# Kernel tuning notes

Hardware: AMD Instinct MI355X
Metric: run time of the kernel (lower is better)

## Reference

```python
import math
import jax, jax.numpy as jnp
import numpy as np

N_HEADS = 16
HIDDEN = 1024
FACTOR = 256
N_DK = HIDDEN // N_HEADS
B, S = 4, 2048


def _linear_params(key, fan_in, fan_out):
    kw, kb = jax.random.split(key)
    bound = 1.0 / math.sqrt(fan_in)
    W = jax.random.uniform(kw, (fan_in, fan_out), jnp.float32, -bound, bound)
    b = jax.random.uniform(kb, (fan_out,), jnp.float32, -bound, bound)
    return W, b


def setup_inputs() -> dict:
    key = jax.random.key(0)
    ks = jax.random.split(key, 12)
    inp = {
        "query": jax.random.normal(ks[0], (B, S, HIDDEN), jnp.float32),
        "key": jax.random.normal(ks[1], (B, S, HIDDEN), jnp.float32),
        "value": jax.random.normal(ks[2], (B, S, HIDDEN), jnp.float32),
        "mask": jax.random.randint(ks[3], (B, S), 0, 2, jnp.int32),
    }
    names = [("pq", HIDDEN, FACTOR), ("tq", FACTOR, HIDDEN),
             ("pk", HIDDEN, FACTOR), ("tk", FACTOR, HIDDEN),
             ("pv", HIDDEN, FACTOR), ("tv", FACTOR, HIDDEN),
             ("po", HIDDEN, FACTOR), ("to", FACTOR, HIDDEN)]
    for i, (nm, fi, fo) in enumerate(names):
        W, b = _linear_params(ks[4 + i], fi, fo)
        inp[f"W{nm}"], inp[f"b{nm}"] = W, b
    return inp


def _factored(x, Wp, bp, Wt, bt):
    # proj -> leaky_relu(0.2) -> tran
    h = jax.nn.leaky_relu(x @ Wp + bp, negative_slope=0.2)
    return h @ Wt + bt


def reference(query, key, value, mask,
              Wpq, bpq, Wtq, btq, Wpk, bpk, Wtk, btk,
              Wpv, bpv, Wtv, btv, Wpo, bpo, Wto, bto):
    bsize = query.shape[0]

    def split_heads(x):  # [B,S,H*Dk] -> [B,H,S,Dk]
        return x.reshape(bsize, -1, N_HEADS, N_DK).transpose(0, 2, 1, 3)

    q = split_heads(_factored(query, Wpq, bpq, Wtq, btq))
    k = split_heads(_factored(key, Wpk, bpk, Wtk, btk))
    v = split_heads(_factored(value, Wpv, bpv, Wtv, btv))

    scores = jnp.einsum("bhqd,bhkd->bhqk", q, k) / math.sqrt(N_DK)
    m = (mask == 0)[:, None, None, :]  # [B,1,1,S]
    scores = jnp.where(m, jnp.float32(-1e20), scores)
    attn = jax.nn.softmax(scores, axis=-1)
    cv = jnp.einsum("bhqk,bhkd->bhqd", attn, v)
    cv = cv.transpose(0, 2, 1, 3).reshape(bsize, -1, N_HEADS * N_DK)
    # dropout omitted (eval mode / deterministic reference)
    return _factored(cv, Wpo, bpo, Wto, bto)
```

## Files before the change

### kernel.cpp

```cpp
#include <hip/hip_runtime.h>
#include <cstdint>
#include <cstddef>

typedef __bf16 bf16_t;
typedef __bf16 bf16x8 __attribute__((ext_vector_type(8)));
typedef float  f32x4  __attribute__((ext_vector_type(4)));
typedef unsigned int uint32x4 __attribute__((ext_vector_type(4)));
typedef unsigned int uint32x2 __attribute__((ext_vector_type(2)));

#define DEV_INLINE __device__ __forceinline__

constexpr int Bsz = 4, Ssz = 2048, HID = 1024, FAC = 256, NH = 16, DKc = 64;
constexpr int Mrows = Bsz * Ssz;
constexpr float QSCALE = 0.18033688011112042f;

struct Ptr8 { const float* p[8]; };
struct Ptr3 { const float* p[3]; };

DEV_INLINE float fast_exp2(float x) {
#if __has_builtin(__builtin_amdgcn_exp2f)
  return __builtin_amdgcn_exp2f(x);
#else
  return exp2f(x);
#endif
}

DEV_INLINE void async16(const void* g, void* l) {
  __builtin_amdgcn_global_load_lds((const __attribute__((address_space(1))) void*)g,
                                   (__attribute__((address_space(3))) void*)l, 16, 0, 0);
}

DEV_INLINE int SW(int r) { return (r & 3) | ((r >> 1) & 4); }

__global__ __launch_bounds__(256) void k_prep(Ptr8 w, Ptr8 bsrc, const int* __restrict__ mask,
                                              bf16_t* wpt, bf16_t* wtt,
                                              float* bp, float* bt, float* mf, bf16_t* mb) {
  const int z = blockIdx.z;
  if (z == 8) {
    const int bid = blockIdx.y * 32 + blockIdx.x;
    if (bid >= 64) return;
    const int i = bid * 256 + threadIdx.x;
    if (i < 4 * FAC) bp[i] = bsrc.p[i >> 8][i & 255];
    if (i < 4 * HID) bt[i] = bsrc.p[4 + (i >> 10)][i & 1023];
    if (i < Bsz * Ssz) {
      const float m = (mask[i] != 0) ? 1.f : 0.f;
      mf[i] = m;
      mb[i] = (bf16_t)m;
    }
    return;
  }
  const int K = (z < 4) ? HID : FAC;
  const int N = (z < 4) ? FAC : HID;
  if ((int)(blockIdx.x * 32) >= N || (int)(blockIdx.y * 32) >= K) return;
  __shared__ float t[32][33];
  const float* src = w.p[z];
  bf16_t* dst = (z < 4) ? (wpt + (size_t)z * FAC * HID) : (wtt + (size_t)(z - 4) * FAC * HID);
  const int tx = threadIdx.x & 31, ty = threadIdx.x >> 5;
  const int kb = blockIdx.y * 32, nb = blockIdx.x * 32;
#pragma unroll
  for (int j = 0; j < 4; ++j)
    t[ty + j * 8][tx] = src[(size_t)(kb + ty + j * 8) * N + nb + tx];
  __syncthreads();
#pragma unroll
  for (int j = 0; j < 4; ++j)
    dst[(size_t)(nb + ty + j * 8) * K + kb + tx] = (bf16_t)t[tx][ty + j * 8];
}

template <int CAST_A, typename OUT_T>
__global__ __launch_bounds__(256) void k_gemmP(Ptr3 Asrc,
                                               const bf16_t* __restrict__ Aall,
                                               const bf16_t* __restrict__ Bt_,
                                               const float* __restrict__ biasAll,
                                               OUT_T* __restrict__ Call,
                                               int K,
                                               long long Az, long long Bz, long long Cz, int biasz) {
  constexpr int LDTA = CAST_A ? 40 : 32;
  __shared__ __align__(16) bf16_t As[2][64 * LDTA];
  __shared__ __align__(16) bf16_t Bs[2][128 * 32];

  const int z = blockIdx.z;
  const bf16_t* Bt = Bt_ + (size_t)z * Bz;
  const float* bias = biasAll + (size_t)z * biasz;
  OUT_T* C = Call + (size_t)z * Cz;

  const int tid = threadIdx.x;
  const int lane = tid & 63, wave = tid >> 6;
  const int quad = lane >> 4, l16 = lane & 15;
  const int m0 = blockIdx.y * 64, n0 = blockIdx.x * 128;

  const int arow = wave * 16 + (lane >> 2), akc = (lane & 3) * 8;
  const bf16_t* gB0 = Bt + (size_t)(n0 + arow) * K + akc;
  const bf16_t* gB1 = gB0 + (size_t)64 * K;

  const float* gAf = nullptr;
  const bf16_t* gA = nullptr;
  const int crow = tid >> 2, chalf = (tid & 3) * 8;
  if (CAST_A) gAf = Asrc.p[z] + (size_t)(m0 + crow) * K + chalf;
  else        gA  = Aall + (size_t)z * Az + (size_t)(m0 + arow) * K + akc;

  async16(gB0, Bs[0] + wave * 512);
  async16(gB1, Bs[0] + 2048 + wave * 512);
  if (CAST_A) {
    f32x4 x0 = *(const f32x4*)gAf;
    f32x4 x1 = *(const f32x4*)(gAf + 4);
    union { bf16_t h[8]; uint32x4 u; } o;
#pragma unroll
    for (int j = 0; j < 4; ++j) { o.h[j] = (bf16_t)x0[j]; o.h[4 + j] = (bf16_t)x1[j]; }
    *(uint32x4*)(As[0] + crow * LDTA + chalf) = o.u;
  } else {
    async16(gA, As[0] + wave * 512);
  }

  f32x4 acc[4][2] = {};
  const int nk = K / 32;

  for (int it = 0; it < nk; ++it) {
    const int cur = it & 1, nxt = cur ^ 1;
    __syncthreads();

    f32x4 xa, xb;
    const int k1 = (it + 1) * 32;
    if (it + 1 < nk) {
      async16(gB0 + k1, Bs[nxt] + wave * 512);
      async16(gB1 + k1, Bs[nxt] + 2048 + wave * 512);
      if (CAST_A) {
        xa = *(const f32x4*)(gAf + k1);
        xb = *(const f32x4*)(gAf + k1 + 4);
      } else {
        async16(gA + k1, As[nxt] + wave * 512);
      }
    }

    bf16x8 af[4], bfr[2];
#pragma unroll
    for (int i = 0; i < 4; ++i)
      af[i] = *(const bf16x8*)(As[cur] + (i * 16 + l16) * LDTA + quad * 8);
#pragma unroll
    for (int i = 0; i < 2; ++i)
      bfr[i] = *(const bf16x8*)(Bs[cur] + (wave * 32 + i * 16 + l16) * 32 + quad * 8);
#pragma unroll
    for (int mi = 0; mi < 4; ++mi)
#pragma unroll
      for (int ni = 0; ni < 2; ++ni)
        acc[mi][ni] = __builtin_amdgcn_mfma_f32_16x16x32_bf16(af[mi], bfr[ni], acc[mi][ni], 0, 0, 0);

    if (CAST_A && it + 1 < nk) {
      union { bf16_t h[8]; uint32x4 u; } o;
#pragma unroll
      for (int j = 0; j < 4; ++j) { o.h[j] = (bf16_t)xa[j]; o.h[4 + j] = (bf16_t)xb[j]; }
      *(uint32x4*)(As[nxt] + crow * LDTA + chalf) = o.u;
    }
  }

#pragma unroll
  for (int mi = 0; mi < 4; ++mi) {
    const int rbase = m0 + mi * 16 + quad * 4;
#pragma unroll
    for (int ni = 0; ni < 2; ++ni) {
      const int col = n0 + wave * 32 + ni * 16 + l16;
      const float bv = bias[col];
#pragma unroll
      for (int r = 0; r < 4; ++r) {
        float y = acc[mi][ni][r] + bv;
        y = (y > 0.f) ? y : 0.2f * y;
        C[(size_t)(rbase + r) * FAC + col] = (OUT_T)y;
      }
    }
  }
}

template <int TVW, typename OUT_T>
__global__ __launch_bounds__(256) void k_gemm(const bf16_t* __restrict__ Aall,
                                              const bf16_t* __restrict__ Btall,
                                              const float* __restrict__ biasAll,
                                              OUT_T* __restrict__ Call,
                                              bf16_t* __restrict__ C2,
                                              const float* __restrict__ rowmul,
                                              int N, int K,
                                              long long Az, long long Bz, long long Cz, int biasz,
                                              float sc0, float sc1) {
  __shared__ __align__(16) bf16_t As[2][128 * 32];
  __shared__ __align__(16) bf16_t Bs[2][128 * 32];

  const int z = blockIdx.z;
  const bf16_t* Bt = Btall + (size_t)z * Bz;
  const float* bias = biasAll + (size_t)z * biasz;
  OUT_T* C = Call + (size_t)z * Cz;
  const float scale = (z == 0) ? sc0 : sc1;

  const int tid = threadIdx.x;
  const int lane = tid & 63, wave = tid >> 6;
  const int quad = lane >> 4, l16 = lane & 15;
  const int wr = wave >> 1, wc = wave & 1;
  const int m0 = blockIdx.y * 128, n0 = blockIdx.x * 128;

  const int arow = wave * 16 + (lane >> 2), akc = (lane & 3) * 8;
  const bf16_t* gB0 = Bt + (size_t)(n0 + arow) * K + akc;
  const bf16_t* gB1 = gB0 + (size_t)64 * K;
  const bf16_t* A = Aall + (size_t)z * Az;
  const bf16_t* gA0 = A + (size_t)(m0 + arow) * K + akc;
  const bf16_t* gA1 = gA0 + (size_t)64 * K;

  async16(gB0, Bs[0] + wave * 512);
  async16(gB1, Bs[0] + 2048 + wave * 512);
  async16(gA0, As[0] + wave * 512);
  async16(gA1, As[0] + 2048 + wave * 512);

  f32x4 acc[4][4] = {};
  const int nk = K / 32;

  for (int it = 0; it < nk; ++it) {
    const int cur = it & 1, nxt = cur ^ 1;
    __syncthreads();

    if (it + 1 < nk) {
      const int k1 = (it + 1) * 32;
      async16(gB0 + k1, Bs[nxt] + wave * 512);
      async16(gB1 + k1, Bs[nxt] + 2048 + wave * 512);
      async16(gA0 + k1, As[nxt] + wave * 512);
      async16(gA1 + k1, As[nxt] + 2048 + wave * 512);
    }

    bf16x8 af[4], bfr[4];
#pragma unroll
    for (int i = 0; i < 4; ++i)
      af[i] = *(const bf16x8*)(As[cur] + (wr * 64 + i * 16 + l16) * 32 + quad * 8);
#pragma unroll
    for (int i = 0; i < 4; ++i)
      bfr[i] = *(const bf16x8*)(Bs[cur] + (wc * 64 + i * 16 + l16) * 32 + quad * 8);
#pragma unroll
    for (int mi = 0; mi < 4; ++mi)
#pragma unroll
      for (int ni = 0; ni < 4; ++ni)
        acc[mi][ni] = __builtin_amdgcn_mfma_f32_16x16x32_bf16(af[mi], bfr[ni], acc[mi][ni], 0, 0, 0);
  }

  if (TVW && z == 2) {
#pragma unroll
    for (int mi = 0; mi < 4; ++mi) {
      const int rbase = m0 + wr * 64 + mi * 16 + quad * 4;
      const int bb = rbase >> 11, s = rbase & 2047;
      float rmv[4];
#pragma unroll
      for (int r = 0; r < 4; ++r) rmv[r] = rowmul[rbase + r];
#pragma unroll
      for (int ni = 0; ni < 4; ++ni) {
        const int col = n0 + wc * 64 + ni * 16 + l16;
        const float bv = bias[col];
        const int h = col >> 6, d = col & 63;
        union { bf16_t e[4]; uint32x2 u; } p;
#pragma unroll
        for (int r = 0; r < 4; ++r) p.e[r] = (bf16_t)((acc[mi][ni][r] + bv) * rmv[r]);
        *(uint32x2*)(C2 + (((size_t)((bb * NH + h) * DKc + d)) << 11) + s) = p.u;
      }
    }
    return;
  }

#pragma unroll
  for (int mi = 0; mi < 4; ++mi) {
    const int rbase = m0 + wr * 64 + mi * 16 + quad * 4;
#pragma unroll
    for (int ni = 0; ni < 4; ++ni) {
      const int col = n0 + wc * 64 + ni * 16 + l16;
      const float bv = bias[col];
#pragma unroll
      for (int r = 0; r < 4; ++r) {
        float y = (acc[mi][ni][r] + bv) * scale;
        C[(size_t)(rbase + r) * N + col] = (OUT_T)y;
      }
    }
  }
}

__global__ __launch_bounds__(512, 4) void k_attn(const bf16_t* __restrict__ qkv,
                                                 const bf16_t* __restrict__ mb,
                                                 bf16_t* __restrict__ cv) {
  __shared__ __align__(16) bf16_t Ks[2][64 * 64];
  __shared__ __align__(16) bf16_t Vt[2][64 * 64];
  __shared__ __align__(16) bf16_t Ml[Ssz];

  const int qt = blockIdx.x, h = blockIdx.y, b = blockIdx.z;
  const bf16_t* qp = qkv;
  const bf16_t* kp = qkv + (size_t)Mrows * HID;
  const bf16_t* vtp = qkv + 2 * (size_t)Mrows * HID + (size_t)(b * NH + h) * DKc * Ssz;

  const int tid = threadIdx.x;
  const int lane = tid & 63, wave = tid >> 6;
  const int quad = lane >> 4, l16 = lane & 15;

  const int r0 = wave * 8 + (lane >> 3);
  const int c0 = ((lane & 7) ^ SW(r0)) * 8;
  const int ldsOff = wave * 512;
  const bf16_t* kgA = kp + (size_t)(b * Ssz + r0) * HID + h * DKc + c0;
  const bf16_t* vgA = vtp + (size_t)r0 * Ssz + c0;

  *(uint32x2*)(Ml + tid * 4) = *(const uint32x2*)(mb + (size_t)b * Ssz + tid * 4);
  async16(kgA, Ks[0] + ldsOff);
  async16(vgA, Vt[0] + ldsOff);

  bf16x8 aq0[2], aq1[2];
#pragma unroll
  for (int g = 0; g < 2; ++g) {
    const size_t qrow = (size_t)(b * Ssz + qt * 256 + g * 128 + wave * 16 + l16) * HID + h * DKc + quad * 8;
    aq0[g] = *(const bf16x8*)(qp + qrow);
    aq1[g] = *(const bf16x8*)(qp + qrow + 32);
  }
  __syncthreads();

  const int krow = 8 * (l16 >> 2) + (l16 & 3);
  f32x4 acc[2][4] = {};
  f32x4 dacc[2] = {};
  const bf16x8 zfrag = {};

  for (int kt = 0; kt < 32; ++kt) {
    const int cur = kt & 1, nxt = cur ^ 1;
    if (kt < 31) {
      const size_t ko = (size_t)(kt + 1) * 64 * HID;
      const int vo = (kt + 1) * 64;
      async16(kgA + ko, Ks[nxt] + ldsOff);
      async16(vgA + vo, Vt[nxt] + ldsOff);
    }

    union U { uint32x4 u; bf16x8 h; } ap0[2], ap1[2];
    constexpr int koff[4] = {0, 4, 32, 36};
#pragma unroll
    for (int ks = 0; ks < 4; ++ks) {
      const int row = krow + koff[ks];
      const int sw = SW(row);
      bf16x8 a0 = *(const bf16x8*)(Ks[cur] + row * 64 + (quad ^ sw) * 8);
      bf16x8 a1 = *(const bf16x8*)(Ks[cur] + row * 64 + ((quad + 4) ^ sw) * 8);
#pragma unroll
      for (int g = 0; g < 2; ++g) {
        f32x4 c = {};
        c = __builtin_amdgcn_mfma_f32_16x16x32_bf16(a0, aq0[g], c, 0, 0, 0);
        c = __builtin_amdgcn_mfma_f32_16x16x32_bf16(a1, aq1[g], c, 0, 0, 0);
        union { bf16_t h[2]; uint32_t u; } p01, p23;
        p01.h[0] = (bf16_t)fast_exp2(c[0]);
        p01.h[1] = (bf16_t)fast_exp2(c[1]);
        p23.h[0] = (bf16_t)fast_exp2(c[2]);
        p23.h[1] = (bf16_t)fast_exp2(c[3]);
        U& t = (ks < 2) ? ap0[g] : ap1[g];
        t.u[(ks & 1) * 2] = p01.u;
        t.u[(ks & 1) * 2 + 1] = p23.u;
      }
    }

    bf16x8 mr0 = *(const bf16x8*)(Ml + kt * 64 + quad * 8);
    bf16x8 mr1 = *(const bf16x8*)(Ml + kt * 64 + 32 + quad * 8);
    if (l16 != 0) { mr0 = zfrag; mr1 = zfrag; }
#pragma unroll
    for (int g = 0; g < 2; ++g) {
      dacc[g] = __builtin_amdgcn_mfma_f32_16x16x32_bf16(ap0[g].h, mr0, dacc[g], 0, 0, 0);
      dacc[g] = __builtin_amdgcn_mfma_f32_16x16x32_bf16(ap1[g].h, mr1, dacc[g], 0, 0, 0);
    }

#pragma unroll
    for (int d = 0; d < 4; ++d) {
      const int row = d * 16 + l16;
      const int sw = SW(row);
      bf16x8 bv0 = *(const bf16x8*)(Vt[cur] + row * 64 + (quad ^ sw) * 8);
      bf16x8 bv1 = *(const bf16x8*)(Vt[cur] + row * 64 + ((quad + 4) ^ sw) * 8);
#pragma unroll
      for (int g = 0; g < 2; ++g) {
        acc[g][d] = __builtin_amdgcn_mfma_f32_16x16x32_bf16(ap0[g].h, bv0, acc[g][d], 0, 0, 0);
        acc[g][d] = __builtin_amdgcn_mfma_f32_16x16x32_bf16(ap1[g].h, bv1, acc[g][d], 0, 0, 0);
      }
    }

    __syncthreads();
  }

#pragma unroll
  for (int g = 0; g < 2; ++g) {
    const size_t obase = (size_t)(b * Ssz + qt * 256 + g * 128 + wave * 16 + quad * 4) * HID + h * DKc + l16;
#pragma unroll
    for (int r = 0; r < 4; ++r) {
      const float denom = __shfl(dacc[g][r], lane & 48, 64);
      const float rl = 1.f / denom;
#pragma unroll
      for (int d = 0; d < 4; ++d)
        cv[obase + (size_t)r * HID + d * 16] = (bf16_t)(acc[g][d][r] * rl);
    }
  }
}

extern "C" void kernel_launch(void* const* d_in, const int* in_sizes, int n_in,
                              void* d_out, int out_size, void* d_ws, size_t ws_size,
                              hipStream_t stream) {
  (void)in_sizes; (void)n_in; (void)out_size; (void)ws_size;
  const float* q_in = (const float*)d_in[0];
  const float* k_in = (const float*)d_in[1];
  const float* v_in = (const float*)d_in[2];
  const int* mask = (const int*)d_in[3];

  bf16_t* XB = (bf16_t*)d_ws;
  bf16_t* H3 = XB + (size_t)3 * Mrows * HID;
  bf16_t* CV = H3 + (size_t)3 * Mrows * FAC;
  bf16_t* WPT = CV + (size_t)Mrows * HID;
  bf16_t* WTT = WPT + (size_t)4 * FAC * HID;
  float* BP = (float*)(WTT + (size_t)4 * FAC * HID);
  float* BT = BP + 4 * FAC;
  float* MF = BT + 4 * HID;
  bf16_t* MB = (bf16_t*)(MF + Mrows);
  bf16_t* VTg = XB + 2 * (size_t)Mrows * HID;

  Ptr8 w;
  w.p[0] = (const float*)d_in[4];  w.p[1] = (const float*)d_in[8];
  w.p[2] = (const float*)d_in[12]; w.p[3] = (const float*)d_in[16];
  w.p[4] = (const float*)d_in[6];  w.p[5] = (const float*)d_in[10];
  w.p[6] = (const float*)d_in[14]; w.p[7] = (const float*)d_in[18];
  Ptr8 bs;
  bs.p[0] = (const float*)d_in[5];  bs.p[1] = (const float*)d_in[9];
  bs.p[2] = (const float*)d_in[13]; bs.p[3] = (const float*)d_in[17];
  bs.p[4] = (const float*)d_in[7];  bs.p[5] = (const float*)d_in[11];
  bs.p[6] = (const float*)d_in[15]; bs.p[7] = (const float*)d_in[19];
  hipLaunchKernelGGL(k_prep, dim3(32, 32, 9), dim3(256), 0, stream, w, bs, mask,
                     WPT, WTT, BP, BT, MF, MB);

  Ptr3 xs; xs.p[0] = q_in; xs.p[1] = k_in; xs.p[2] = v_in;
  Ptr3 nullp; nullp.p[0] = nullp.p[1] = nullp.p[2] = nullptr;

  hipLaunchKernelGGL((k_gemmP<1, bf16_t>), dim3(2, Mrows / 64, 3), dim3(256), 0, stream,
                     xs, (const bf16_t*)nullptr, WPT, BP, H3,
                     HID, 0LL, (long long)FAC * HID, (long long)Mrows * FAC, FAC);

  hipLaunchKernelGGL((k_gemm<1, bf16_t>), dim3(HID / 128, Mrows / 128, 3), dim3(256), 0, stream,
                     H3, WTT, BT, XB, VTg, MF,
                     HID, FAC, (long long)Mrows * FAC, (long long)FAC * HID, (long long)Mrows * HID, HID,
                     QSCALE, 1.f);

  hipLaunchKernelGGL(k_attn, dim3(Ssz / 256, NH, Bsz), dim3(512), 0, stream, XB, MB, CV);

  hipLaunchKernelGGL((k_gemmP<0, bf16_t>), dim3(2, Mrows / 64, 1), dim3(256), 0, stream,
                     nullp, CV, WPT + (size_t)3 * FAC * HID, BP + 3 * FAC, H3,
                     HID, 0LL, 0LL, 0LL, 0);

  hipLaunchKernelGGL((k_gemm<0, float>), dim3(HID / 128, Mrows / 128, 1), dim3(256), 0, stream,
                     H3, WTT + (size_t)3 * FAC * HID, BT + 3 * HID, (float*)d_out, (bf16_t*)nullptr,
                     (const float*)nullptr, HID, FAC, 0LL, 0LL, 0LL, 0, 1.f, 1.f);
}
```

Measured before the change: 340.6 us.

## Split attention key tiles across two wave teams with LDS reduction

Waves are now split into two teams. Each team handles half of every 64-key tile (32 keys) for all 64 query rows, where previously each wave covered 32 query rows across the full key tile. At the end, team 1 writes its partial accumulators and denominators to a new LDS scratch buffer, and team 0 adds them and writes the normalized output. The aim is to halve the per-wave K fragment loads and exp work per query row, and to change register usage. The cost is more accumulator registers, extra LDS (about 20KB), and a final reduction with several barriers, which could lower occupancy.

After: 656.0 us. 92.6% more time.

```diff
diff --git a/kernel.cpp b/kernel.cpp
--- a/kernel.cpp
+++ b/kernel.cpp
@@ -279,6 +279,7 @@
   __shared__ __align__(16) bf16_t Ks[2][64 * 64];
   __shared__ __align__(16) bf16_t Vt[2][64 * 64];
   __shared__ __align__(16) bf16_t Ml[Ssz];
+  __shared__ __align__(16) float scr[256 * 20];
 
   const int qt = blockIdx.x, h = blockIdx.y, b = blockIdx.z;
   const bf16_t* qp = qkv;
@@ -288,6 +289,7 @@
   const int tid = threadIdx.x;
   const int lane = tid & 63, wave = tid >> 6;
   const int quad = lane >> 4, l16 = lane & 15;
+  const int team = wave >> 2, w4 = wave & 3;
 
   const int r0 = wave * 8 + (lane >> 3);
   const int c0 = ((lane & 7) ^ SW(r0)) * 8;
@@ -299,18 +301,18 @@
   async16(kgA, Ks[0] + ldsOff);
   async16(vgA, Vt[0] + ldsOff);
 
-  bf16x8 aq0[2], aq1[2];
-#pragma unroll
-  for (int g = 0; g < 2; ++g) {
-    const size_t qrow = (size_t)(b * Ssz + qt * 256 + g * 128 + wave * 16 + l16) * HID + h * DKc + quad * 8;
+  bf16x8 aq0[4], aq1[4];
+#pragma unroll
+  for (int g = 0; g < 4; ++g) {
+    const size_t qrow = (size_t)(b * Ssz + qt * 256 + g * 64 + w4 * 16 + l16) * HID + h * DKc + quad * 8;
     aq0[g] = *(const bf16x8*)(qp + qrow);
     aq1[g] = *(const bf16x8*)(qp + qrow + 32);
   }
   __syncthreads();
 
   const int krow = 8 * (l16 >> 2) + (l16 & 3);
-  f32x4 acc[2][4] = {};
-  f32x4 dacc[2] = {};
+  f32x4 acc[4][4] = {};
+  f32x4 dacc[4] = {};
   const bf16x8 zfrag = {};
 
   for (int kt = 0; kt < 32; ++kt) {
@@ -322,16 +324,15 @@
       async16(vgA + vo, Vt[nxt] + ldsOff);
     }
 
-    union U { uint32x4 u; bf16x8 h; } ap0[2], ap1[2];
-    constexpr int koff[4] = {0, 4, 32, 36};
-#pragma unroll
-    for (int ks = 0; ks < 4; ++ks) {
-      const int row = krow + koff[ks];
+    union U { uint32x4 u; bf16x8 h; } ap[4];
+#pragma unroll
+    for (int ks = 0; ks < 2; ++ks) {
+      const int row = krow + ks * 4 + team * 32;
       const int sw = SW(row);
       bf16x8 a0 = *(const bf16x8*)(Ks[cur] + row * 64 + (quad ^ sw) * 8);
       bf16x8 a1 = *(const bf16x8*)(Ks[cur] + row * 64 + ((quad + 4) ^ sw) * 8);
 #pragma unroll
-      for (int g = 0; g < 2; ++g) {
+      for (int g = 0; g < 4; ++g) {
         f32x4 c = {};
         c = __builtin_amdgcn_mfma_f32_16x16x32_bf16(a0, aq0[g], c, 0, 0, 0);
         c = __builtin_amdgcn_mfma_f32_16x16x32_bf16(a1, aq1[g], c, 0, 0, 0);
@@ -340,48 +341,53 @@
         p01.h[1] = (bf16_t)fast_exp2(c[1]);
         p23.h[0] = (bf16_t)fast_exp2(c[2]);
         p23.h[1] = (bf16_t)fast_exp2(c[3]);
-        U& t = (ks < 2) ? ap0[g] : ap1[g];
-        t.u[(ks & 1) * 2] = p01.u;
-        t.u[(ks & 1) * 2 + 1] = p23.u;
-      }
-    }
-
-    bf16x8 mr0 = *(const bf16x8*)(Ml + kt * 64 + quad * 8);
-    bf16x8 mr1 = *(const bf16x8*)(Ml + kt * 64 + 32 + quad * 8);
-    if (l16 != 0) { mr0 = zfrag; mr1 = zfrag; }
-#pragma unroll
-    for (int g = 0; g < 2; ++g) {
-      dacc[g] = __builtin_amdgcn_mfma_f32_16x16x32_bf16(ap0[g].h, mr0, dacc[g], 0, 0, 0);
-      dacc[g] = __builtin_amdgcn_mfma_f32_16x16x32_bf16(ap1[g].h, mr1, dacc[g], 0, 0, 0);
-    }
+        ap[g].u[ks * 2] = p01.u;
+        ap[g].u[ks * 2 + 1] = p23.u;
+      }
+    }
+
+    bf16x8 mr = *(const bf16x8*)(Ml + kt * 64 + team * 32 + quad * 8);
+    if (l16 != 0) mr = zfrag;
+#pragma unroll
+    for (int g = 0; g < 4; ++g)
+      dacc[g] = __builtin_amdgcn_mfma_f32_16x16x32_bf16(ap[g].h, mr, dacc[g], 0, 0, 0);
 
 #pragma unroll
     for (int d = 0; d < 4; ++d) {
       const int row = d * 16 + l16;
       const int sw = SW(row);
-      bf16x8 bv0 = *(const bf16x8*)(Vt[cur] + row * 64 + (quad ^ sw) * 8);
-      bf16x8 bv1 = *(const bf16x8*)(Vt[cur] + row * 64 + ((quad + 4) ^ sw) * 8);
-#pragma unroll
-      for (int g = 0; g < 2; ++g) {
-        acc[g][d] = __builtin_amdgcn_mfma_f32_16x16x32_bf16(ap0[g].h, bv0, acc[g][d], 0, 0, 0);
-        acc[g][d] = __builtin_amdgcn_mfma_f32_16x16x32_bf16(ap1[g].h, bv1, acc[g][d], 0, 0, 0);
-      }
+      bf16x8 bv = *(const bf16x8*)(Vt[cur] + row * 64 + (((quad + team * 4)) ^ sw) * 8);
+#pragma unroll
+      for (int g = 0; g < 4; ++g)
+        acc[g][d] = __builtin_amdgcn_mfma_f32_16x16x32_bf16(ap[g].h, bv, acc[g][d], 0, 0, 0);
     }
 
     __syncthreads();
   }
 
-#pragma unroll
-  for (int g = 0; g < 2; ++g) {
-    const size_t obase = (size_t)(b * Ssz + qt * 256 + g * 128 + wave * 16 + quad * 4) * HID + h * DKc + l16;
-#pragma unroll
-    for (int r = 0; r < 4; ++r) {
-      const float denom = __shfl(dacc[g][r], lane & 48, 64);
-      const float rl = 1.f / denom;
-#pragma unroll
-      for (int d = 0; d < 4; ++d)
-        cv[obase + (size_t)r * HID + d * 16] = (bf16_t)(acc[g][d][r] * rl);
-    }
+  const int sbase = (w4 * 64 + lane) * 20;
+  for (int g = 0; g < 4; ++g) {
+    if (team == 1) {
+#pragma unroll
+      for (int d = 0; d < 4; ++d) *(f32x4*)(scr + sbase + d * 4) = acc[g][d];
+      *(f32x4*)(scr + sbase + 16) = dacc[g];
+    }
+    __syncthreads();
+    if (team == 0) {
+#pragma unroll
+      for (int d = 0; d < 4; ++d) acc[g][d] += *(const f32x4*)(scr + sbase + d * 4);
+      dacc[g] += *(const f32x4*)(scr + sbase + 16);
+      const size_t obase = (size_t)(b * Ssz + qt * 256 + g * 64 + w4 * 16 + quad * 4) * HID + h * DKc + l16;
+#pragma unroll
+      for (int r = 0; r < 4; ++r) {
+        const float denom = __shfl(dacc[g][r], lane & 48, 64);
+        const float rl = 1.f / denom;
+#pragma unroll
+        for (int d = 0; d < 4; ++d)
+          cv[obase + (size_t)r * HID + d * 16] = (bf16_t)(acc[g][d][r] * rl);
+      }
+    }
+    __syncthreads();
   }
 }
 
```

## Fuse factored proj and tran GEMMs into one kernel keeping hidden tile in LDS

Applied to the files above, without the earlier changes.

Replaces the separate projection GEMM (K=1024 to 256) and transform GEMM (256 to 1024) with one 512-thread kernel per 64-row tile. The leaky-ReLU intermediate stays in shared memory and is never written to or read back from global memory, and the launch count drops from four GEMM launches to two. In exchange each block computes all 1024 output columns serially in 32 chunks. The grid shrinks to 128 blocks per z, which lowers parallelism, and the larger LDS footprint may reduce occupancy.

Result: no change. 343.7 us (+0.9%).

```diff
diff --git a/kernel.cpp b/kernel.cpp
--- a/kernel.cpp
+++ b/kernel.cpp
@@ -66,211 +66,183 @@
     dst[(size_t)(nb + ty + j * 8) * K + kb + tx] = (bf16_t)t[tx][ty + j * 8];
 }
 
-template <int CAST_A, typename OUT_T>
-__global__ __launch_bounds__(256) void k_gemmP(Ptr3 Asrc,
-                                               const bf16_t* __restrict__ Aall,
-                                               const bf16_t* __restrict__ Bt_,
-                                               const float* __restrict__ biasAll,
-                                               OUT_T* __restrict__ Call,
-                                               int K,
-                                               long long Az, long long Bz, long long Cz, int biasz) {
+template <int CAST_A, int QKV, typename OUT_T>
+__global__ __launch_bounds__(512, 4) void k_fact(Ptr3 Asrc, const bf16_t* __restrict__ Abf,
+                                                 const bf16_t* __restrict__ WpAll,
+                                                 const float* __restrict__ bpAll,
+                                                 const bf16_t* __restrict__ WtAll,
+                                                 const float* __restrict__ btAll,
+                                                 OUT_T* __restrict__ CoutAll,
+                                                 bf16_t* __restrict__ C2,
+                                                 const float* __restrict__ rowmul) {
   constexpr int LDTA = CAST_A ? 40 : 32;
-  __shared__ __align__(16) bf16_t As[2][64 * LDTA];
-  __shared__ __align__(16) bf16_t Bs[2][128 * 32];
-
-  const int z = blockIdx.z;
-  const bf16_t* Bt = Bt_ + (size_t)z * Bz;
-  const float* bias = biasAll + (size_t)z * biasz;
-  OUT_T* C = Call + (size_t)z * Cz;
+  __shared__ __align__(16) bf16_t smem[2 * 64 * 40 + 2 * 256 * 32 + 64 * 264];
+  bf16_t* As  = smem;
+  bf16_t* Bs1 = smem + 2 * 64 * 40;
+  bf16_t* Bs2 = smem;
+  bf16_t* Hl  = smem + 2 * 64 * 40 + 2 * 256 * 32;
+
+  const int z = QKV ? blockIdx.z : 3;
+  const bf16_t* Wp = WpAll + (size_t)z * FAC * HID;
+  const float* bp = bpAll + z * FAC;
+  const bf16_t* Wt = WtAll + (size_t)z * FAC * HID;
+  const float* bt = btAll + z * HID;
+  OUT_T* Cout = QKV ? (CoutAll + (size_t)blockIdx.z * Mrows * HID) : CoutAll;
 
   const int tid = threadIdx.x;
   const int lane = tid & 63, wave = tid >> 6;
   const int quad = lane >> 4, l16 = lane & 15;
-  const int m0 = blockIdx.y * 64, n0 = blockIdx.x * 128;
-
-  const int arow = wave * 16 + (lane >> 2), akc = (lane & 3) * 8;
-  const bf16_t* gB0 = Bt + (size_t)(n0 + arow) * K + akc;
-  const bf16_t* gB1 = gB0 + (size_t)64 * K;
-
+  const int m0 = blockIdx.x * 64;
+
+  const int b1row = wave * 32 + (lane >> 2), b1col = (lane & 3) * 8;
+  const bf16_t* gW0 = Wp + (size_t)b1row * HID + b1col;
+  const bf16_t* gW1 = gW0 + (size_t)16 * HID;
+  bf16_t* lW0 = Bs1 + wave * 1024;
+  bf16_t* lW1 = lW0 + 512;
+
+  const int ar = tid >> 3, acf = (tid & 7) * 4;
   const float* gAf = nullptr;
-  const bf16_t* gA = nullptr;
-  const int crow = tid >> 2, chalf = (tid & 3) * 8;
-  if (CAST_A) gAf = Asrc.p[z] + (size_t)(m0 + crow) * K + chalf;
-  else        gA  = Aall + (size_t)z * Az + (size_t)(m0 + arow) * K + akc;
-
-  async16(gB0, Bs[0] + wave * 512);
-  async16(gB1, Bs[0] + 2048 + wave * 512);
+  const bf16_t* gAb = nullptr;
+  bf16_t* lA = As + wave * 512;
+  if (CAST_A) gAf = Asrc.p[z] + (size_t)(m0 + ar) * HID + acf;
+  else        gAb = Abf + (size_t)(m0 + wave * 16 + (lane >> 2)) * HID + (lane & 3) * 8;
+
+  async16(gW0, lW0);
+  async16(gW1, lW1);
   if (CAST_A) {
-    f32x4 x0 = *(const f32x4*)gAf;
-    f32x4 x1 = *(const f32x4*)(gAf + 4);
-    union { bf16_t h[8]; uint32x4 u; } o;
-#pragma unroll
-    for (int j = 0; j < 4; ++j) { o.h[j] = (bf16_t)x0[j]; o.h[4 + j] = (bf16_t)x1[j]; }
-    *(uint32x4*)(As[0] + crow * LDTA + chalf) = o.u;
-  } else {
-    async16(gA, As[0] + wave * 512);
+    f32x4 x = *(const f32x4*)gAf;
+    union { bf16_t h[4]; uint32x2 u; } o;
+#pragma unroll
+    for (int j = 0; j < 4; ++j) o.h[j] = (bf16_t)x[j];
+    *(uint32x2*)(As + ar * LDTA + acf) = o.u;
+  } else if (wave < 4) {
+    async16(gAb, lA);
   }
 
   f32x4 acc[4][2] = {};
-  const int nk = K / 32;
-
-  for (int it = 0; it < nk; ++it) {
+
+  for (int it = 0; it < 32; ++it) {
     const int cur = it & 1, nxt = cur ^ 1;
     __syncthreads();
 
-    f32x4 xa, xb;
-    const int k1 = (it + 1) * 32;
-    if (it + 1 < nk) {
-      async16(gB0 + k1, Bs[nxt] + wave * 512);
-      async16(gB1 + k1, Bs[nxt] + 2048 + wave * 512);
-      if (CAST_A) {
-        xa = *(const f32x4*)(gAf + k1);
-        xb = *(const f32x4*)(gAf + k1 + 4);
-      } else {
-        async16(gA + k1, As[nxt] + wave * 512);
-      }
+    f32x4 xa = {};
+    if (it + 1 < 32) {
+      const int k1 = (it + 1) * 32;
+      async16(gW0 + k1, lW0 + nxt * 8192);
+      async16(gW1 + k1, lW1 + nxt * 8192);
+      if (CAST_A) xa = *(const f32x4*)(gAf + k1);
+      else if (wave < 4) async16(gAb + k1, lA + nxt * 2048);
     }
 
     bf16x8 af[4], bfr[2];
 #pragma unroll
     for (int i = 0; i < 4; ++i)
-      af[i] = *(const bf16x8*)(As[cur] + (i * 16 + l16) * LDTA + quad * 8);
+      af[i] = *(const bf16x8*)(As + cur * 64 * LDTA + (i * 16 + l16) * LDTA + quad * 8);
 #pragma unroll
     for (int i = 0; i < 2; ++i)
-      bfr[i] = *(const bf16x8*)(Bs[cur] + (wave * 32 + i * 16 + l16) * 32 + quad * 8);
+      bfr[i] = *(const bf16x8*)(Bs1 + cur * 8192 + (wave * 32 + i * 16 + l16) * 32 + quad * 8);
 #pragma unroll
     for (int mi = 0; mi < 4; ++mi)
 #pragma unroll
       for (int ni = 0; ni < 2; ++ni)
         acc[mi][ni] = __builtin_amdgcn_mfma_f32_16x16x32_bf16(af[mi], bfr[ni], acc[mi][ni], 0, 0, 0);
 
-    if (CAST_A && it + 1 < nk) {
-      union { bf16_t h[8]; uint32x4 u; } o;
-#pragma unroll
-      for (int j = 0; j < 4; ++j) { o.h[j] = (bf16_t)xa[j]; o.h[4 + j] = (bf16_t)xb[j]; }
-      *(uint32x4*)(As[nxt] + crow * LDTA + chalf) = o.u;
-    }
-  }
-
-#pragma unroll
-  for (int mi = 0; mi < 4; ++mi) {
-    const int rbase = m0 + mi * 16 + quad * 4;
+    if (CAST_A && it + 1 < 32) {
+      union { bf16_t h[4]; uint32x2 u; } o;
+#pragma unroll
+      for (int j = 0; j < 4; ++j) o.h[j] = (bf16_t)xa[j];
+      *(uint32x2*)(As + nxt * 64 * LDTA + ar * LDTA + acf) = o.u;
+    }
+  }
+
+#pragma unroll
+  for (int mi = 0; mi < 4; ++mi)
 #pragma unroll
     for (int ni = 0; ni < 2; ++ni) {
-      const int col = n0 + wave * 32 + ni * 16 + l16;
-      const float bv = bias[col];
+      const int col = wave * 32 + ni * 16 + l16;
+      const float bv = bp[col];
 #pragma unroll
       for (int r = 0; r < 4; ++r) {
         float y = acc[mi][ni][r] + bv;
         y = (y > 0.f) ? y : 0.2f * y;
-        C[(size_t)(rbase + r) * FAC + col] = (OUT_T)y;
+        Hl[(mi * 16 + quad * 4 + r) * 264 + col] = (bf16_t)y;
       }
-    }
-  }
-}
-
-template <int TVW, typename OUT_T>
-__global__ __launch_bounds__(256) void k_gemm(const bf16_t* __restrict__ Aall,
-                                              const bf16_t* __restrict__ Btall,
-                                              const float* __restrict__ biasAll,
-                                              OUT_T* __restrict__ Call,
-                                              bf16_t* __restrict__ C2,
-                                              const float* __restrict__ rowmul,
-                                              int N, int K,
-                                              long long Az, long long Bz, long long Cz, int biasz,
-                                              float sc0, float sc1) {
-  __shared__ __align__(16) bf16_t As[2][128 * 32];
-  __shared__ __align__(16) bf16_t Bs[2][128 * 32];
-
-  const int z = blockIdx.z;
-  const bf16_t* Bt = Btall + (size_t)z * Bz;
-  const float* bias = biasAll + (size_t)z * biasz;
-  OUT_T* C = Call + (size_t)z * Cz;
-  const float scale = (z == 0) ? sc0 : sc1;
-
-  const int tid = threadIdx.x;
-  const int lane = tid & 63, wave = tid >> 6;
-  const int quad = lane >> 4, l16 = lane & 15;
-  const int wr = wave >> 1, wc = wave & 1;
-  const int m0 = blockIdx.y * 128, n0 = blockIdx.x * 128;
-
-  const int arow = wave * 16 + (lane >> 2), akc = (lane & 3) * 8;
-  const bf16_t* gB0 = Bt + (size_t)(n0 + arow) * K + akc;
-  const bf16_t* gB1 = gB0 + (size_t)64 * K;
-  const bf16_t* A = Aall + (size_t)z * Az;
-  const bf16_t* gA0 = A + (size_t)(m0 + arow) * K + akc;
-  const bf16_t* gA1 = gA0 + (size_t)64 * K;
-
-  async16(gB0, Bs[0] + wave * 512);
-  async16(gB1, Bs[0] + 2048 + wave * 512);
-  async16(gA0, As[0] + wave * 512);
-  async16(gA1, As[0] + 2048 + wave * 512);
-
-  f32x4 acc[4][4] = {};
-  const int nk = K / 32;
-
-  for (int it = 0; it < nk; ++it) {
-    const int cur = it & 1, nxt = cur ^ 1;
+      acc[mi][ni] = (f32x4){0.f, 0.f, 0.f, 0.f};
+    }
+  __syncthreads();
+
+  const int b2row = wave * 32 + (lane >> 2), b2col = (lane & 3) * 8;
+#define STAGE2(ci, buf)                                                                  \
+  {                                                                                      \
+    const int nb_ = ((ci) >> 3) * 256, k0_ = ((ci) & 7) * 32;                            \
+    const bf16_t* g0_ = Wt + (size_t)(nb_ + b2row) * FAC + k0_ + b2col;                  \
+    async16(g0_, Bs2 + (buf) * 8192 + wave * 1024);                                      \
+    async16(g0_ + 16 * FAC, Bs2 + (buf) * 8192 + wave * 1024 + 512);                     \
+  }
+  STAGE2(0, 0);
+
+  for (int ci = 0; ci < 32; ++ci) {
+    const int cur = ci & 1, nxt = cur ^ 1;
     __syncthreads();
-
-    if (it + 1 < nk) {
-      const int k1 = (it + 1) * 32;
-      async16(gB0 + k1, Bs[nxt] + wave * 512);
-      async16(gB1 + k1, Bs[nxt] + 2048 + wave * 512);
-      async16(gA0 + k1, As[nxt] + wave * 512);
-      async16(gA1 + k1, As[nxt] + 2048 + wave * 512);
-    }
-
-    bf16x8 af[4], bfr[4];
+    if (ci + 1 < 32) STAGE2(ci + 1, nxt);
+
+    bf16x8 af[4], bfr[2];
+    const int k0 = (ci & 7) * 32;
 #pragma unroll
     for (int i = 0; i < 4; ++i)
-      af[i] = *(const bf16x8*)(As[cur] + (wr * 64 + i * 16 + l16) * 32 + quad * 8);
-#pragma unroll
-    for (int i = 0; i < 4; ++i)
-      bfr[i] = *(const bf16x8*)(Bs[cur] + (wc * 64 + i * 16 + l16) * 32 + quad * 8);
+      af[i] = *(const bf16x8*)(Hl + (i * 16 + l16) * 264 + k0 + quad * 8);
+#pragma unroll
+    for (int i = 0; i < 2; ++i)
+      bfr[i] = *(const bf16x8*)(Bs2 + cur * 8192 + (wave * 32 + i * 16 + l16) * 32 + quad * 8);
 #pragma unroll
     for (int mi = 0; mi < 4; ++mi)
 #pragma unroll
-      for (int ni = 0; ni < 4; ++ni)
+      for (int ni = 0; ni < 2; ++ni)
         acc[mi][ni] = __builtin_amdgcn_mfma_f32_16x16x32_bf16(af[mi], bfr[ni], acc[mi][ni], 0, 0, 0);
-  }
-
-  if (TVW && z == 2) {
-#pragma unroll
-    for (int mi = 0; mi < 4; ++mi) {
-      const int rbase = m0 + wr * 64 + mi * 16 + quad * 4;
-      const int bb = rbase >> 11, s = rbase & 2047;
-      float rmv[4];
-#pragma unroll
-      for (int r = 0; r < 4; ++r) rmv[r] = rowmul[rbase + r];
-#pragma unroll
-      for (int ni = 0; ni < 4; ++ni) {
-        const int col = n0 + wc * 64 + ni * 16 + l16;
-        const float bv = bias[col];
-        const int h = col >> 6, d = col & 63;
-        union { bf16_t e[4]; uint32x2 u; } p;
-#pragma unroll
-        for (int r = 0; r < 4; ++r) p.e[r] = (bf16_t)((acc[mi][ni][r] + bv) * rmv[r]);
-        *(uint32x2*)(C2 + (((size_t)((bb * NH + h) * DKc + d)) << 11) + s) = p.u;
+
+    if ((ci & 7) == 7) {
+      const int nbase = (ci >> 3) * 256;
+      if (QKV && blockIdx.z == 2) {
+#pragma unroll
+        for (int mi = 0; mi < 4; ++mi) {
+          const int rbase = m0 + mi * 16 + quad * 4;
+          const int bb = rbase >> 11, s = rbase & 2047;
+          float rmv[4];
+#pragma unroll
+          for (int r = 0; r < 4; ++r) rmv[r] = rowmul[rbase + r];
+#pragma unroll
+          for (int ni = 0; ni < 2; ++ni) {
+            const int col = nbase + wave * 32 + ni * 16 + l16;
+            const float bv = bt[col];
+            const int hh = col >> 6, d = col & 63;
+            union { bf16_t e[4]; uint32x2 u; } p;
+#pragma unroll
+            for (int r = 0; r < 4; ++r) p.e[r] = (bf16_t)((acc[mi][ni][r] + bv) * rmv[r]);
+            *(uint32x2*)(C2 + (((size_t)((bb * NH + hh) * DKc + d)) << 11) + s) = p.u;
+          }
+        }
+      } else {
+        const float scale = (QKV && blockIdx.z == 0) ? QSCALE : 1.f;
+#pragma unroll
+        for (int mi = 0; mi < 4; ++mi) {
+          const int row = m0 + mi * 16 + quad * 4;
+#pragma unroll
+          for (int ni = 0; ni < 2; ++ni) {
+            const int col = nbase + wave * 32 + ni * 16 + l16;
+            const float bv = bt[col];
+#pragma unroll
+            for (int r = 0; r < 4; ++r)
+              Cout[(size_t)(row + r) * HID + col] = (OUT_T)((acc[mi][ni][r] + bv) * scale);
+          }
+        }
       }
-    }
-    return;
-  }
-
-#pragma unroll
-  for (int mi = 0; mi < 4; ++mi) {
-    const int rbase = m0 + wr * 64 + mi * 16 + quad * 4;
-#pragma unroll
-    for (int ni = 0; ni < 4; ++ni) {
-      const int col = n0 + wc * 64 + ni * 16 + l16;
-      const float bv = bias[col];
-#pragma unroll
-      for (int r = 0; r < 4; ++r) {
-        float y = (acc[mi][ni][r] + bv) * scale;
-        C[(size_t)(rbase + r) * N + col] = (OUT_T)y;
-      }
-    }
-  }
+#pragma unroll
+      for (int mi = 0; mi < 4; ++mi)
+#pragma unroll
+        for (int ni = 0; ni < 2; ++ni) acc[mi][ni] = (f32x4){0.f, 0.f, 0.f, 0.f};
+    }
+  }
+#undef STAGE2
 }
 
 __global__ __launch_bounds__(512, 4) void k_attn(const bf16_t* __restrict__ qkv,
@@ -421,22 +393,12 @@
   Ptr3 xs; xs.p[0] = q_in; xs.p[1] = k_in; xs.p[2] = v_in;
   Ptr3 nullp; nullp.p[0] = nullp.p[1] = nullp.p[2] = nullptr;
 
-  hipLaunchKernelGGL((k_gemmP<1, bf16_t>), dim3(2, Mrows / 64, 3), dim3(256), 0, stream,
-                     xs, (const bf16_t*)nullptr, WPT, BP, H3,
-                     HID, 0LL, (long long)FAC * HID, (long long)Mrows * FAC, FAC);
-
-  hipLaunchKernelGGL((k_gemm<1, bf16_t>), dim3(HID / 128, Mrows / 128, 3), dim3(256), 0, stream,
-                     H3, WTT, BT, XB, VTg, MF,
-                     HID, FAC, (long long)Mrows * FAC, (long long)FAC * HID, (long long)Mrows * HID, HID,
-                     QSCALE, 1.f);
+  hipLaunchKernelGGL((k_fact<1, 1, bf16_t>), dim3(Mrows / 64, 1, 3), dim3(512), 0, stream,
+                     xs, (const bf16_t*)nullptr, WPT, BP, WTT, BT, XB, VTg, MF);
 
   hipLaunchKernelGGL(k_attn, dim3(Ssz / 256, NH, Bsz), dim3(512), 0, stream, XB, MB, CV);
 
-  hipLaunchKernelGGL((k_gemmP<0, bf16_t>), dim3(2, Mrows / 64, 1), dim3(256), 0, stream,
-                     nullp, CV, WPT + (size_t)3 * FAC * HID, BP + 3 * FAC, H3,
-                     HID, 0LL, 0LL, 0LL, 0);
-
-  hipLaunchKernelGGL((k_gemm<0, float>), dim3(HID / 128, Mrows / 128, 1), dim3(256), 0, stream,
-                     H3, WTT + (size_t)3 * FAC * HID, BT + 3 * HID, (float*)d_out, (bf16_t*)nullptr,
-                     (const float*)nullptr, HID, FAC, 0LL, 0LL, 0LL, 0, 1.f, 1.f);
-}
+  hipLaunchKernelGGL((k_fact<0, 0, float>), dim3(Mrows / 64, 1, 1), dim3(512), 0, stream,
+                     nullp, CV, WPT, BP, WTT, BT, (float*)d_out, (bf16_t*)nullptr,
+                     (const float*)nullptr);
+}
```
